# Kernel tuning notes

Measured on AMD Instinct MI355X. Metric: run time of the kernel, lower is better.

## Reference

```python
import jax, jax.numpy as jnp
import numpy as np

B, S, W, E, H, V, C = 32, 512, 15, 300, 256, 50000, 2
G = 3 * H  # stacked GRU gate dim


def setup_inputs() -> dict:
    key = jax.random.key(0)
    ks = jax.random.split(key, 20)
    f = lambda k, shape, s=0.05: jax.random.normal(k, shape, dtype=jnp.float32) * s
    return {
        "x": jax.random.randint(ks[0], (B, S), 0, V),
        "x_pre": jax.random.randint(ks[1], (B, S), 0, V),
        "x_alt": jax.random.randint(ks[2], (B, S), 0, V),
        "x_cur": jax.random.randint(ks[3], (B, S), 0, V),
        "seq_lens": jax.random.randint(ks[4], (B,), 1, S),
        "emb": f(ks[5], (V, E), 0.1),
        "W_ih_f": f(ks[6], (G, E)), "W_hh_f": f(ks[7], (G, H)),
        "b_ih_f": jnp.zeros((G,), jnp.float32), "b_hh_f": jnp.zeros((G,), jnp.float32),
        "W_ih_b": f(ks[8], (G, E)), "W_hh_b": f(ks[9], (G, H)),
        "b_ih_b": jnp.zeros((G,), jnp.float32), "b_hh_b": jnp.zeros((G,), jnp.float32),
        "bn_gamma": jnp.ones((2 * H,), jnp.float32), "bn_beta": jnp.zeros((2 * H,), jnp.float32),
        "mlp_W": f(ks[10], (2 * H, 2 * H)), "mlp_b": jnp.zeros((2 * H,), jnp.float32),
        "lin_W": f(ks[11], (C, 2 * H)), "lin_b": jnp.zeros((C,), jnp.float32),
    }


def _gru_last(xs, Wih, Whh, bih, bhh, reverse):
    """xs: [T, N, E]; returns final hidden state [N, H] of a torch-style GRU."""
    xp = jnp.einsum('tne,ge->tng', xs, Wih) + bih  # precompute input projections
    h0 = jnp.zeros((xs.shape[1], Whh.shape[1]), xs.dtype)

    def step(h, xg):
        hg = h @ Whh.T + bhh
        xr, xz, xn = jnp.split(xg, 3, axis=-1)
        hr, hz, hn = jnp.split(hg, 3, axis=-1)
        r = jax.nn.sigmoid(xr + hr)
        z = jax.nn.sigmoid(xz + hz)
        n = jnp.tanh(xn + r * hn)
        return (1.0 - z) * n + z * h, None

    h, _ = jax.lax.scan(step, h0, xp, reverse=reverse)
    return h


def reference(x, x_pre, x_alt, x_cur, seq_lens, emb,
              W_ih_f, W_hh_f, b_ih_f, b_hh_f,
              W_ih_b, W_hh_b, b_ih_b, b_hh_b,
              bn_gamma, bn_beta, mlp_W, mlp_b, lin_W, lin_b):
    mask = (x > 0).astype(jnp.float32)[:, :, None]            # [B,S,1]
    idx = jnp.arange(S)[:, None] + jnp.arange(W)[None, :]      # [S,W] window gather
    # torch pads the id tensor with 0 then embeds -> pad rows embed to emb[0]
    ef = emb[jnp.pad(x, ((0, 0), (W - 1, 0)))]                 # [B,S+W-1,E]
    et = emb[jnp.pad(x, ((0, 0), (0, W - 1)))]
    fwin = ef[:, idx].transpose(2, 0, 1, 3).reshape(W, B * S, E)
    twin = et[:, idx].transpose(2, 0, 1, 3).reshape(W, B * S, E)
    hf = _gru_last(fwin, W_ih_f, W_hh_f, b_ih_f, b_hh_f, False).reshape(B, S, H)
    hb = _gru_last(twin, W_ih_b, W_hh_b, b_ih_b, b_hh_b, True).reshape(B, S, H)
    hidden = jnp.concatenate([hf * mask, hb * mask], axis=2)   # [B,S,2H]
    # BatchNorm1d (training-mode batch stats, per channel over B and S)
    mu = hidden.mean(axis=(0, 1))
    var = ((hidden - mu) ** 2).mean(axis=(0, 1))
    normed = ((hidden - mu) / jnp.sqrt(var + 1e-5)) * bn_gamma + bn_beta
    normed = normed * mask
    mlp_h = (normed @ mlp_W.T + mlp_b) * mask + (mask - 1.0) * 65500.0
    pooled = mlp_h.max(axis=1)                                 # [B,2H] masked max-pool
    return pooled @ lin_W.T + lin_b                            # [B,C]
```

## Files before the change

### kernel.cpp

```cpp
#include <hip/hip_runtime.h>
#include <hip/hip_bf16.h>
#include <stdint.h>


typedef unsigned short u16;
typedef unsigned int u32;
typedef float f32x16 __attribute__((ext_vector_type(16)));
typedef float f32x4  __attribute__((ext_vector_type(4)));
typedef short bf16x8 __attribute__((ext_vector_type(8)));

#define MFMA32 __builtin_amdgcn_mfma_f32_32x32x16_bf16
#define MFMA16 __builtin_amdgcn_mfma_f32_16x16x32_bf16

#define NB 32
#define NS 512
#define NW 15
#define NE 300
#define NH 256
#define NG 768
#define NCELL (NB*NS)
#define EPAD 320
#define MRE 32
#define MRR 64
#define HS 264
#define WROWS 78
#define RZS 260
#define NSS 264

__device__ __forceinline__ float bf2f(u16 u){
    union { unsigned int i; float f; } v; v.i = ((unsigned int)u) << 16; return v.f;
}
__device__ __forceinline__ u16 f2bf(float f){
    union { float f; unsigned int i; } v; v.f = f;
    unsigned int x = v.i;
    x += 0x7fffu + ((x >> 16) & 1u);
    return (u16)(x >> 16);
}
__device__ __forceinline__ u16 f2bf_rh(float f){
    return (u16)((__float_as_uint(f) + 0x8000u) >> 16);
}
__device__ __forceinline__ unsigned fkey(float f){
    unsigned b = __float_as_uint(f);
    return b ^ ((b & 0x80000000u) ? 0xFFFFFFFFu : 0x80000000u);
}

__device__ __forceinline__ float sigm_hw(float x){
    return __builtin_amdgcn_rcpf(1.0f + __builtin_amdgcn_exp2f(x * -1.44269504f));
}
__device__ __forceinline__ float tanh_hw(float x){
    return fmaf(-2.0f, __builtin_amdgcn_rcpf(1.0f + __builtin_amdgcn_exp2f(x * 2.88539008f)), 1.0f);
}

__global__ void prep_kernel(const float* __restrict__ Wih_f, const float* __restrict__ Wih_b,
                            const float* __restrict__ Whh_f, const float* __restrict__ Whh_b,
                            const float* __restrict__ mlpW,
                            u16* __restrict__ WihF_p, u16* __restrict__ WihB_p,
                            u16* __restrict__ WhhF_p, u16* __restrict__ WhhB_p,
                            u16* __restrict__ mlpW_p,
                            float* __restrict__ bnSum, float* __restrict__ bnSumSq,
                            unsigned* __restrict__ pooled_u)
{
    const int tid  = blockIdx.x*blockDim.x + threadIdx.x;
    const int nthr = gridDim.x*blockDim.x;
    for (int i = tid; i < 3*8*20*64; i += nthr){
        const int lane = i & 63;
        const int t2   = i >> 6;
        const int kc   = t2 % 20;
        const int wvg  = t2 / 20;
        const int g    = wvg >> 3, wv = wvg & 7;
        const int col  = wv*32 + (lane & 31);
        const int k0   = kc*16 + (lane >> 5)*8;
        const float* sF = Wih_f + (size_t)(g*NH + col)*NE;
        const float* sB = Wih_b + (size_t)(g*NH + col)*NE;
        u16* dF = WihF_p + (size_t)i*8;
        u16* dB = WihB_p + (size_t)i*8;
        #pragma unroll
        for (int j = 0; j < 8; j++){
            const int k = k0 + j;
            dF[j] = (k < NE) ? f2bf(sF[k]) : (u16)0;
            dB[j] = (k < NE) ? f2bf(sB[k]) : (u16)0;
        }
    }
    for (int i = tid; i < 3*16*8*64; i += nthr){
        const int lane = i & 63;
        const int kc   = (i >> 6) & 7;
        const int wvg  = i >> 9;
        const int g    = wvg >> 4, wv = wvg & 15;
        const int l15  = lane & 15, q = lane >> 4;
        const int col  = wv*16 + l15;
        const int k0   = kc*32 + q*8;
        const float* srcF = Whh_f + (size_t)(g*NH + col)*NH + k0;
        const float* srcB = Whh_b + (size_t)(g*NH + col)*NH + k0;
        u16* dF = WhhF_p + (size_t)i*8;
        u16* dB = WhhB_p + (size_t)i*8;
        #pragma unroll
        for (int j = 0; j < 8; j++){ dF[j] = f2bf(srcF[j]); dB[j] = f2bf(srcB[j]); }
    }
    for (int i = tid; i < 2*8*32*64; i += nthr){
        const int lane = i & 63;
        const int t2   = i >> 6;
        const int kc   = t2 & 31;
        const int ntwv = t2 >> 5;
        const int nt   = ntwv >> 3, wv = ntwv & 7;
        const int row  = wv*64 + nt*32 + (lane & 31);
        const int k0   = kc*16 + (lane >> 5)*8;
        const float* s = mlpW + (size_t)row*512 + k0;
        u16* d = mlpW_p + (size_t)i*8;
        #pragma unroll
        for (int j = 0; j < 8; j++) d[j] = f2bf(s[j]);
    }
    for (int i = tid; i < 512; i += nthr){ bnSum[i] = 0.0f; bnSumSq[i] = 0.0f; }
    for (int i = tid; i < NB*512; i += nthr) pooled_u[i] = 0u;
}

__global__ __launch_bounds__(512, 4)
void eproj_kernel(const int* __restrict__ x, const float* __restrict__ emb,
                  const u16* __restrict__ WihF_p, const u16* __restrict__ WihB_p,
                  const float* __restrict__ bih_f, const float* __restrict__ bhh_f,
                  const float* __restrict__ bih_b, const float* __restrict__ bhh_b,
                  u32* __restrict__ rzF, u16* __restrict__ nF,
                  u32* __restrict__ rzB, u16* __restrict__ nB)
{
    __shared__ u16 a_lds[MRE*328];
    const int tid = threadIdx.x;
    const int dir = (blockIdx.x >= 514);
    const int mb  = dir ? (blockIdx.x - 514) : blockIdx.x;
    const u16* Wih_p = dir ? WihB_p : WihF_p;
    const float* b_ih = dir ? bih_b : bih_f;
    const float* b_hh = dir ? bhh_b : bhh_f;
    u32* xprojRZ = dir ? rzB : rzF;
    u16* xprojN  = dir ? nB  : nF;
    {
        const int row = tid >> 4, jj = tid & 15;
        const int flat = mb*MRE + row;
        const int t_id = (flat < NCELL) ? x[flat] : 0;
        const float4* src = (const float4*)(emb + (size_t)t_id*NE);
        u16* dst = a_lds + row*328;
        for (int idx = jj; idx < 75; idx += 16){
            float4 v = src[idx];
            ushort4 o; o.x=f2bf(v.x); o.y=f2bf(v.y); o.z=f2bf(v.z); o.w=f2bf(v.w);
            *(ushort4*)(dst + idx*4) = o;
        }
        if (jj == 15){
            const ushort4 z = {0,0,0,0};
            #pragma unroll
            for (int c = 300; c < 320; c += 4) *(ushort4*)(dst + c) = z;
        }
    }
    __syncthreads();

    const int lane = tid & 63, wv = tid >> 6, l31 = lane & 31, q = lane >> 5;
    const int col = wv*32 + l31;
    f32x16 acc[3];
    #pragma unroll
    for (int g = 0; g < 3; g++)
        #pragma unroll
        for (int i = 0; i < 16; i++) acc[g][i] = 0.0f;

    const u16* a0p = a_lds + l31*328 + q*8;
    const char* wf0 = (const char*)Wih_p + (size_t)((0*8 + wv)*20)*1024 + (size_t)lane*16;
    const char* wf1 = (const char*)Wih_p + (size_t)((1*8 + wv)*20)*1024 + (size_t)lane*16;
    const char* wf2 = (const char*)Wih_p + (size_t)((2*8 + wv)*20)*1024 + (size_t)lane*16;

    #pragma unroll 4
    for (int kc = 0; kc < 20; kc++){
        bf16x8 a0 = *(const bf16x8*)(a0p + kc*16);
        bf16x8 b0 = *(const bf16x8*)(wf0 + kc*1024);
        bf16x8 b1 = *(const bf16x8*)(wf1 + kc*1024);
        bf16x8 b2 = *(const bf16x8*)(wf2 + kc*1024);
        acc[0] = MFMA32(a0,b0,acc[0],0,0,0);
        acc[1] = MFMA32(a0,b1,acc[1],0,0,0);
        acc[2] = MFMA32(a0,b2,acc[2],0,0,0);
    }
    const float br  = b_ih[col]      + b_hh[col];
    const float bz  = b_ih[NH+col]   + b_hh[NH+col];
    const float bn_ = b_ih[2*NH+col];
    #pragma unroll
    for (int r = 0; r < 16; r++){
        const int rit = (r&3) + 8*(r>>2) + 4*q;
        const int row = mb*MRE + rit;
        const u32 rzv = (u32)f2bf(acc[0][r] + br) | ((u32)f2bf(acc[1][r] + bz) << 16);
        xprojRZ[(size_t)row*256 + col] = rzv;
        xprojN [(size_t)row*256 + col] = f2bf(acc[2][r] + bn_);
    }
}

__global__ __launch_bounds__(1024, 4)
void recur_kernel(const int* __restrict__ x,
                  const u32* __restrict__ rzF, const u16* __restrict__ nF,
                  const u32* __restrict__ rzB, const u16* __restrict__ nB,
                  const u16* __restrict__ WhhF_p, const u16* __restrict__ WhhB_p,
                  const float* __restrict__ bhh_f, const float* __restrict__ bhh_b,
                  u16* __restrict__ hidden, float* __restrict__ bnSum, float* __restrict__ bnSumSq)
{
    __shared__ u32 rz_lds[WROWS*RZS];
    __shared__ u16 n_lds [WROWS*NSS];
    __shared__ u16 h_lds [MRR*HS];
    __shared__ float maskv[MRR];
    const int tid = threadIdx.x;
    const int bid = blockIdx.x & 255;
    const int dir = blockIdx.x >> 8;
    const u32* xprojRZ = dir ? rzB : rzF;
    const u16* xprojN  = dir ? nB  : nF;
    const u16* Whh_p   = dir ? WhhB_p : WhhF_p;
    const float* b_hh  = dir ? bhh_b : bhh_f;
    const int mb  = ((bid & 7) << 5) | (bid >> 3);
    if (tid < MRR) maskv[tid] = (x[mb*MRR + tid] > 0) ? 1.0f : 0.0f;

    const int bidx = (mb*MRR) >> 9;
    const int s0   = (mb*MRR) & (NS-1);
    const int joff = s0 + (dir ? 0 : -(NW-1));

    for (int i = tid; i < WROWS*64; i += 1024){
        const int w = i >> 6, c4 = i & 63;
        const int j = joff + w;
        const size_t row = ((unsigned)j < (unsigned)NS) ? (size_t)(bidx*NS + j) : (size_t)NCELL;
        const uint4 v = *(const uint4*)(xprojRZ + row*256 + c4*4);
        *(uint4*)(rz_lds + w*RZS + c4*4) = v;
    }
    for (int i = tid; i < WROWS*32; i += 1024){
        const int w = i >> 5, c8 = i & 31;
        const int j = joff + w;
        const size_t row = ((unsigned)j < (unsigned)NS) ? (size_t)(bidx*NS + j) : (size_t)NCELL;
        const uint4 v = *(const uint4*)(xprojN + row*256 + c8*8);
        *(uint4*)(n_lds + w*NSS + c8*8) = v;
    }
    __syncthreads();

    const int lane = tid & 63, wv = tid >> 6;
    const int l15 = lane & 15, q = lane >> 4;
    const int col  = wv*16 + l15;

    const float bhn = b_hh[2*NH + col];

    const char* wf = (const char*)Whh_p + ((size_t)wv << 13) + ((size_t)lane << 4);

    const int haOff = l15*HS + q*8;
    const u32* rzp0 = rz_lds + q*4*RZS + col;
    const u16* nnp0 = n_lds  + q*4*NSS + col;

    float hreg[16];
    #pragma unroll
    for (int i = 0; i < 16; i++) hreg[i] = 0.0f;

    #pragma unroll 1
    for (int t = 0; t < NW; t++){
        f32x4 acc[4][3];
        #pragma unroll
        for (int mt = 0; mt < 4; mt++)
            #pragma unroll
            for (int g = 0; g < 3; g++)
                #pragma unroll
                for (int i = 0; i < 4; i++) acc[mt][g][i] = (g == 2) ? bhn : 0.0f;

        if (t > 0){
            const u16* hcur = h_lds + haOff;
            bf16x8 b0 = *(const bf16x8*)(wf + 0*131072);
            bf16x8 b1 = *(const bf16x8*)(wf + 1*131072);
            bf16x8 b2 = *(const bf16x8*)(wf + 2*131072);
            #pragma unroll
            for (int kc = 0; kc < 8; kc++){
                bf16x8 n0, n1, n2;
                if (kc < 7){
                    const int ko = (kc+1)*1024;
                    n0 = *(const bf16x8*)(wf + 0*131072 + ko);
                    n1 = *(const bf16x8*)(wf + 1*131072 + ko);
                    n2 = *(const bf16x8*)(wf + 2*131072 + ko);
                }
                bf16x8 a0 = *(const bf16x8*)(hcur + kc*32 +   0);
                bf16x8 a1 = *(const bf16x8*)(hcur + kc*32 + 16*HS);
                bf16x8 a2 = *(const bf16x8*)(hcur + kc*32 + 32*HS);
                bf16x8 a3 = *(const bf16x8*)(hcur + kc*32 + 48*HS);
                acc[0][0] = MFMA16(a0,b0,acc[0][0],0,0,0);
                acc[1][0] = MFMA16(a1,b0,acc[1][0],0,0,0);
                acc[2][0] = MFMA16(a2,b0,acc[2][0],0,0,0);
                acc[3][0] = MFMA16(a3,b0,acc[3][0],0,0,0);
                acc[0][1] = MFMA16(a0,b1,acc[0][1],0,0,0);
                acc[1][1] = MFMA16(a1,b1,acc[1][1],0,0,0);
                acc[2][1] = MFMA16(a2,b1,acc[2][1],0,0,0);
                acc[3][1] = MFMA16(a3,b1,acc[3][1],0,0,0);
                acc[0][2] = MFMA16(a0,b2,acc[0][2],0,0,0);
                acc[1][2] = MFMA16(a1,b2,acc[1][2],0,0,0);
                acc[2][2] = MFMA16(a2,b2,acc[2][2],0,0,0);
                acc[3][2] = MFMA16(a3,b2,acc[3][2],0,0,0);
                if (kc < 7){ b0 = n0; b1 = n1; b2 = n2; }
            }
        }
        const int wbase = (dir == 0) ? t : ((NW-1) - t);
        const u32* rzp = rzp0 + wbase*RZS;
        const u16* nnp = nnp0 + wbase*NSS;
        #pragma unroll
        for (int half = 0; half < 2; half++){
            u32 rz[8]; u16 nn[8];
            #pragma unroll
            for (int i = 0; i < 8; i++){
                const int ii = half*8 + i;
                const int mt = ii >> 2, r = ii & 3;
                rz[i] = rzp[(mt*16 + r)*RZS];
                nn[i] = nnp[(mt*16 + r)*NSS];
            }
            #pragma unroll
            for (int i = 0; i < 8; i++){
                const int ii = half*8 + i;
                const int mt = ii >> 2, r = ii & 3;
                const float xr = bf2f((u16)(rz[i] & 0xFFFFu));
                const float xz = bf2f((u16)(rz[i] >> 16));
                const float xn = bf2f(nn[i]);
                const float rg = sigm_hw(xr + acc[mt][0][r]);
                const float zg = sigm_hw(xz + acc[mt][1][r]);
                const float ng = tanh_hw(fmaf(rg, acc[mt][2][r], xn));
                hreg[ii] = fmaf(zg, hreg[ii] - ng, ng);
            }
        }
        if (t + 1 < NW){
            __syncthreads();
            #pragma unroll
            for (int mt = 0; mt < 4; mt++)
                #pragma unroll
                for (int r = 0; r < 4; r++){
                    const int rit = mt*16 + q*4 + r;
                    h_lds[rit*HS + col] = f2bf_rh(hreg[mt*4 + r]);
                }
            __syncthreads();
        }
    }
    float sum = 0.0f, sumsq = 0.0f;
    #pragma unroll
    for (int mt = 0; mt < 4; mt++)
        #pragma unroll
        for (int r = 0; r < 4; r++){
            const int rit = mt*16 + q*4 + r;
            const float hm = hreg[mt*4 + r] * maskv[rit];
            hidden[(size_t)(mb*MRR + rit)*512 + dir*NH + col] = f2bf(hm);
            sum += hm; sumsq += hm*hm;
        }
    sum   += __shfl_xor(sum, 16);   sumsq += __shfl_xor(sumsq, 16);
    sum   += __shfl_xor(sum, 32);   sumsq += __shfl_xor(sumsq, 32);
    if (q == 0){
        atomicAdd(&bnSum[dir*NH + col], sum);
        atomicAdd(&bnSumSq[dir*NH + col], sumsq);
    }
}

__global__ void bnfin_kernel(const float* __restrict__ bnSum, const float* __restrict__ bnSumSq,
                             const float* __restrict__ gamma, const float* __restrict__ beta,
                             float* __restrict__ bnScale, float* __restrict__ bnShift)
{
    const int c = blockIdx.x*blockDim.x + threadIdx.x;
    if (c < 512){
        const float mu  = bnSum[c]   * (1.0f/16384.0f);
        const float var = bnSumSq[c] * (1.0f/16384.0f) - mu*mu;
        const float inv = rsqrtf(var + 1e-5f);
        const float sc  = gamma[c]*inv;
        bnScale[c] = sc;
        bnShift[c] = beta[c] - mu*sc;
    }
}

__global__ __launch_bounds__(512, 4)
void mlp_kernel(const int* __restrict__ x, const u16* __restrict__ hidden,
                const u16* __restrict__ mlpW_p, const float* __restrict__ bnScale,
                const float* __restrict__ bnShift, const float* __restrict__ mlp_b,
                unsigned* __restrict__ pooled_u)
{
    __shared__ u16 a_lds[MRE*520];
    __shared__ float maskv[MRE];
    const int tid = threadIdx.x;
    const int mb  = blockIdx.x;
    if (tid < MRE) maskv[tid] = (x[mb*MRE + tid] > 0) ? 1.0f : 0.0f;
    __syncthreads();
    {
        const int row = tid >> 4, jj = tid & 15;
        const float m = maskv[row];
        const u16* src = hidden + (size_t)(mb*MRE + row)*512;
        u16* dst = a_lds + row*520;
        for (int c4 = jj; c4 < 128; c4 += 16){
            ushort4 v = ((const ushort4*)src)[c4];
            const int c = c4*4;
            float4 sc = *(const float4*)(bnScale + c);
            float4 sh = *(const float4*)(bnShift + c);
            ushort4 o;
            o.x = f2bf((bf2f(v.x)*sc.x + sh.x)*m);
            o.y = f2bf((bf2f(v.y)*sc.y + sh.y)*m);
            o.z = f2bf((bf2f(v.z)*sc.z + sh.z)*m);
            o.w = f2bf((bf2f(v.w)*sc.w + sh.w)*m);
            *(ushort4*)(dst + c) = o;
        }
    }
    __syncthreads();

    const int lane = tid & 63, wv = tid >> 6, l31 = lane & 31, q = lane >> 5;
    f32x16 acc[2];
    #pragma unroll
    for (int g = 0; g < 2; g++)
        #pragma unroll
        for (int i = 0; i < 16; i++) acc[g][i] = 0.0f;

    const u16* a0p = a_lds + l31*520 + q*8;
    const char* wm0 = (const char*)mlpW_p + (size_t)((0*8 + wv)*32)*1024 + (size_t)lane*16;
    const char* wm1 = (const char*)mlpW_p + (size_t)((1*8 + wv)*32)*1024 + (size_t)lane*16;

    #pragma unroll 4
    for (int kc = 0; kc < 32; kc++){
        bf16x8 a0 = *(const bf16x8*)(a0p + kc*16);
        bf16x8 b0 = *(const bf16x8*)(wm0 + kc*1024);
        bf16x8 b1 = *(const bf16x8*)(wm1 + kc*1024);
        acc[0] = MFMA32(a0,b0,acc[0],0,0,0);
        acc[1] = MFMA32(a0,b1,acc[1],0,0,0);
    }

    const int bidx = mb >> 4;
    #pragma unroll
    for (int nt = 0; nt < 2; nt++){
        const int colg = wv*64 + nt*32 + l31;
        const float bias = mlp_b[colg];
        float mx = -3.4e38f;
        #pragma unroll
        for (int r = 0; r < 16; r++){
            const int rit = (r&3) + 8*(r>>2) + 4*q;
            const float m = maskv[rit];
            const float v = (acc[nt][r] + bias)*m + (m - 1.0f)*65500.0f;
            mx = fmaxf(mx, v);
        }
        mx = fmaxf(mx, __shfl_xor(mx, 32));
        if (q == 0) atomicMax(&pooled_u[bidx*512 + colg], fkey(mx));
    }
}

__global__ void final_kernel(const unsigned* __restrict__ pooled_u,
                             const float* __restrict__ linW, const float* __restrict__ linb,
                             float* __restrict__ out)
{
    const int b = blockIdx.x;
    const int lane = threadIdx.x;
    float s0 = 0.0f, s1 = 0.0f;
    for (int c = lane; c < 512; c += 64){
        const unsigned u = pooled_u[b*512 + c];
        const unsigned bits = (u & 0x80000000u) ? (u ^ 0x80000000u) : ~u;
        const float f = __uint_as_float(bits);
        s0 += f * linW[c];
        s1 += f * linW[512 + c];
    }
    #pragma unroll
    for (int off = 32; off > 0; off >>= 1){
        s0 += __shfl_xor(s0, off);
        s1 += __shfl_xor(s1, off);
    }
    if (lane == 0){ out[2*b] = s0 + linb[0]; out[2*b + 1] = s1 + linb[1]; }
}

extern "C" void kernel_launch(void* const* d_in, const int* in_sizes, int n_in,
                              void* d_out, int out_size, void* d_ws, size_t ws_size,
                              hipStream_t stream)
{
    const int*   x     = (const int*)  d_in[0];
    const float* emb   = (const float*)d_in[5];
    const float* Wih_f = (const float*)d_in[6];
    const float* Whh_f = (const float*)d_in[7];
    const float* bih_f = (const float*)d_in[8];
    const float* bhh_f = (const float*)d_in[9];
    const float* Wih_b = (const float*)d_in[10];
    const float* Whh_b = (const float*)d_in[11];
    const float* bih_b = (const float*)d_in[12];
    const float* bhh_b = (const float*)d_in[13];
    const float* gamma = (const float*)d_in[14];
    const float* beta  = (const float*)d_in[15];
    const float* mlpW  = (const float*)d_in[16];
    const float* mlpb  = (const float*)d_in[17];
    const float* linW  = (const float*)d_in[18];
    const float* linb  = (const float*)d_in[19];
    float* out = (float*)d_out;
    char* ws = (char*)d_ws;

    u16*   WihF_p  = (u16*)  (ws + 0);
    u16*   WihB_p  = (u16*)  (ws + 491520);
    u16*   WhhF_p  = (u16*)  (ws + 983040);
    u16*   WhhB_p  = (u16*)  (ws + 1376256);
    u16*   mlpW_p  = (u16*)  (ws + 1769472);
    float* bnSum   = (float*)(ws + 2293760);
    float* bnSumSq = (float*)(ws + 2295808);
    float* bnScale = (float*)(ws + 2297856);
    float* bnShift = (float*)(ws + 2299904);
    unsigned* pooled_u = (unsigned*)(ws + 2301952);
    u16*   hidden  = (u16*)  (ws + 2367488);
    u32*   rzF     = (u32*)  (ws + 19144704);
    u16*   nF      = (u16*)  (ws + 35987456);
    u32*   rzB     = (u32*)  (ws + 44408832);
    u16*   nB      = (u16*)  (ws + 61251584);

    prep_kernel<<<512, 256, 0, stream>>>(Wih_f, Wih_b, Whh_f, Whh_b, mlpW,
                                         WihF_p, WihB_p, WhhF_p, WhhB_p, mlpW_p,
                                         bnSum, bnSumSq, pooled_u);
    eproj_kernel<<<1028, 512, 0, stream>>>(x, emb, WihF_p, WihB_p,
                                           bih_f, bhh_f, bih_b, bhh_b,
                                           rzF, nF, rzB, nB);
    recur_kernel<<<512, 1024, 0, stream>>>(x, rzF, nF, rzB, nB,
                                           WhhF_p, WhhB_p, bhh_f, bhh_b,
                                           hidden, bnSum, bnSumSq);

    bnfin_kernel<<<2, 256, 0, stream>>>(bnSum, bnSumSq, gamma, beta, bnScale, bnShift);
    mlp_kernel<<<512, 512, 0, stream>>>(x, hidden, mlpW_p, bnScale, bnShift, mlpb, pooled_u);
    final_kernel<<<32, 64, 0, stream>>>(pooled_u, linW, linb, out);
}
```

Measured before the change: 465.7 us.

## Prefetch recurrent weights across timesteps and write hidden state inline

The recurrent loop now issues loads of the first two k-chunks of W_hh at the end of each timestep, so they overlap with the next step's barrier. Inside the loop it prefetches two chunks ahead instead of one. The barriers move to bracket the MFMA phase, so each new h value is written to LDS as soon as the gate math produces it rather than in a separate pass. Bf16-to-float conversion is done with shifts and masks. This adds register pressure from the extra prefetched operands.

Result: slower. 608.6 us (+30.7%).

```diff
diff --git a/kernel.cpp b/kernel.cpp
--- a/kernel.cpp
+++ b/kernel.cpp
@@ -243,6 +243,8 @@
     #pragma unroll
     for (int i = 0; i < 16; i++) hreg[i] = 0.0f;
 
+    bf16x8 p00, p01, p02, p10, p11, p12;
+
     #pragma unroll 1
     for (int t = 0; t < NW; t++){
         f32x4 acc[4][3];
@@ -254,41 +256,42 @@
                 for (int i = 0; i < 4; i++) acc[mt][g][i] = (g == 2) ? bhn : 0.0f;
 
         if (t > 0){
+            __syncthreads();
             const u16* hcur = h_lds + haOff;
-            bf16x8 b0 = *(const bf16x8*)(wf + 0*131072);
-            bf16x8 b1 = *(const bf16x8*)(wf + 1*131072);
-            bf16x8 b2 = *(const bf16x8*)(wf + 2*131072);
+            bf16x8 c0 = p00, c1 = p01, c2 = p02;
+            bf16x8 n0 = p10, n1 = p11, n2 = p12;
             #pragma unroll
             for (int kc = 0; kc < 8; kc++){
-                bf16x8 n0, n1, n2;
-                if (kc < 7){
-                    const int ko = (kc+1)*1024;
+                bf16x8 a0 = *(const bf16x8*)(hcur + kc*32 +   0);
+                bf16x8 a1 = *(const bf16x8*)(hcur + kc*32 + 16*HS);
+                bf16x8 a2 = *(const bf16x8*)(hcur + kc*32 + 32*HS);
+                bf16x8 a3 = *(const bf16x8*)(hcur + kc*32 + 48*HS);
+                acc[0][0] = MFMA16(a0,c0,acc[0][0],0,0,0);
+                acc[1][0] = MFMA16(a1,c0,acc[1][0],0,0,0);
+                acc[2][0] = MFMA16(a2,c0,acc[2][0],0,0,0);
+                acc[3][0] = MFMA16(a3,c0,acc[3][0],0,0,0);
+                acc[0][1] = MFMA16(a0,c1,acc[0][1],0,0,0);
+                acc[1][1] = MFMA16(a1,c1,acc[1][1],0,0,0);
+                acc[2][1] = MFMA16(a2,c1,acc[2][1],0,0,0);
+                acc[3][1] = MFMA16(a3,c1,acc[3][1],0,0,0);
+                acc[0][2] = MFMA16(a0,c2,acc[0][2],0,0,0);
+                acc[1][2] = MFMA16(a1,c2,acc[1][2],0,0,0);
+                acc[2][2] = MFMA16(a2,c2,acc[2][2],0,0,0);
+                acc[3][2] = MFMA16(a3,c2,acc[3][2],0,0,0);
+                c0 = n0; c1 = n1; c2 = n2;
+                if (kc < 6){
+                    const int ko = (kc+2)*1024;
                     n0 = *(const bf16x8*)(wf + 0*131072 + ko);
                     n1 = *(const bf16x8*)(wf + 1*131072 + ko);
                     n2 = *(const bf16x8*)(wf + 2*131072 + ko);
                 }
-                bf16x8 a0 = *(const bf16x8*)(hcur + kc*32 +   0);
-                bf16x8 a1 = *(const bf16x8*)(hcur + kc*32 + 16*HS);
-                bf16x8 a2 = *(const bf16x8*)(hcur + kc*32 + 32*HS);
-                bf16x8 a3 = *(const bf16x8*)(hcur + kc*32 + 48*HS);
-                acc[0][0] = MFMA16(a0,b0,acc[0][0],0,0,0);
-                acc[1][0] = MFMA16(a1,b0,acc[1][0],0,0,0);
-                acc[2][0] = MFMA16(a2,b0,acc[2][0],0,0,0);
-                acc[3][0] = MFMA16(a3,b0,acc[3][0],0,0,0);
-                acc[0][1] = MFMA16(a0,b1,acc[0][1],0,0,0);
-                acc[1][1] = MFMA16(a1,b1,acc[1][1],0,0,0);
-                acc[2][1] = MFMA16(a2,b1,acc[2][1],0,0,0);
-                acc[3][1] = MFMA16(a3,b1,acc[3][1],0,0,0);
-                acc[0][2] = MFMA16(a0,b2,acc[0][2],0,0,0);
-                acc[1][2] = MFMA16(a1,b2,acc[1][2],0,0,0);
-                acc[2][2] = MFMA16(a2,b2,acc[2][2],0,0,0);
-                acc[3][2] = MFMA16(a3,b2,acc[3][2],0,0,0);
-                if (kc < 7){ b0 = n0; b1 = n1; b2 = n2; }
             }
+            __syncthreads();
         }
         const int wbase = (dir == 0) ? t : ((NW-1) - t);
         const u32* rzp = rzp0 + wbase*RZS;
         const u16* nnp = nnp0 + wbase*NSS;
+        const bool dowr = (t + 1 < NW);
         #pragma unroll
         for (int half = 0; half < 2; half++){
             u32 rz[8]; u16 nn[8];
@@ -303,26 +306,25 @@
             for (int i = 0; i < 8; i++){
                 const int ii = half*8 + i;
                 const int mt = ii >> 2, r = ii & 3;
-                const float xr = bf2f((u16)(rz[i] & 0xFFFFu));
-                const float xz = bf2f((u16)(rz[i] >> 16));
-                const float xn = bf2f(nn[i]);
+                const float xr = __uint_as_float(rz[i] << 16);
+                const float xz = __uint_as_float(rz[i] & 0xffff0000u);
+                const float xn = __uint_as_float(((u32)nn[i]) << 16);
                 const float rg = sigm_hw(xr + acc[mt][0][r]);
                 const float zg = sigm_hw(xz + acc[mt][1][r]);
                 const float ng = tanh_hw(fmaf(rg, acc[mt][2][r], xn));
                 hreg[ii] = fmaf(zg, hreg[ii] - ng, ng);
+                if (dowr){
+                    const int rit = mt*16 + q*4 + r;
+                    h_lds[rit*HS + col] = f2bf_rh(hreg[ii]);
+                }
             }
         }
-        if (t + 1 < NW){
-            __syncthreads();
-            #pragma unroll
-            for (int mt = 0; mt < 4; mt++)
-                #pragma unroll
-                for (int r = 0; r < 4; r++){
-                    const int rit = mt*16 + q*4 + r;
-                    h_lds[rit*HS + col] = f2bf_rh(hreg[mt*4 + r]);
-                }
-            __syncthreads();
-        }
+        p00 = *(const bf16x8*)(wf + 0*131072);
+        p01 = *(const bf16x8*)(wf + 1*131072);
+        p02 = *(const bf16x8*)(wf + 2*131072);
+        p10 = *(const bf16x8*)(wf + 0*131072 + 1024);
+        p11 = *(const bf16x8*)(wf + 1*131072 + 1024);
+        p12 = *(const bf16x8*)(wf + 2*131072 + 1024);
     }
     float sum = 0.0f, sumsq = 0.0f;
     #pragma unroll
```
